# Performance work log

Hardware: AMD Instinct MI355X
Metric: run time of the kernel (lower is better)

## Reference

```python
import jax, jax.numpy as jnp
import numpy as np

N = 100000   # nodes
E = 640000   # edges
G = 256      # graphs in batch
L = 3        # mpnn layers
D_IN = 64    # in_node_channels
E_IN = 16    # in_edge_channels
H = 128      # hidden width (uniform)


def setup_inputs() -> dict:
    key = jax.random.key(0)
    ks = jax.random.split(key, 20)
    s = 0.05
    inp = {
        "x": jax.random.normal(ks[0], (N, D_IN), dtype=jnp.float32),
        "edge_index": jax.random.randint(ks[1], (2, E), 0, N, dtype=jnp.int64),
        "edge_attr": jax.random.normal(ks[2], (E, E_IN), dtype=jnp.float32),
        "batch_vec": jnp.sort(jax.random.randint(ks[3], (N,), 0, G, dtype=jnp.int64)),
        # input encoders
        "Wn0": jax.random.normal(ks[4], (D_IN, H), dtype=jnp.float32) * s,
        "bn0": jnp.zeros((H,), jnp.float32),
        "We0": jax.random.normal(ks[5], (E_IN, H), dtype=jnp.float32) * s,
        "be0": jnp.zeros((H,), jnp.float32),
        # per-layer MPNN params (stacked over L)
        "WM": jax.random.normal(ks[6], (L, 3 * H, H), dtype=jnp.float32) * s,
        "bM": jnp.zeros((L, H), jnp.float32),
        "WU": jax.random.normal(ks[7], (L, 2 * H, H), dtype=jnp.float32) * s,
        "bU": jnp.zeros((L, H), jnp.float32),
        # per-layer node/edge linear layers
        "Wn": jax.random.normal(ks[8], (L, H, H), dtype=jnp.float32) * s,
        "bn": jnp.zeros((L, H), jnp.float32),
        "We": jax.random.normal(ks[9], (L, H, H), dtype=jnp.float32) * s,
        "be": jnp.zeros((L, H), jnp.float32),
        "Wh": jax.random.normal(ks[10], (H, 1), dtype=jnp.float32) * s,
        "bh": jnp.zeros((1,), jnp.float32),
    }
    return inp


def _mpnn_layer(x, edge_attr, src, dst, WM, bM, WU, bU):
    # message: relu(Linear([x_i, x_j, e]))  (x_i = target, x_j = source)
    xi = x[dst]                                   # [E, H]
    xj = x[src]                                   # [E, H]
    m = jax.nn.relu(jnp.concatenate([xi, xj, edge_attr], axis=-1) @ WM + bM)
    # mean aggregation at target nodes
    agg = jax.ops.segment_sum(m, dst, num_segments=N)        # [N, H]
    cnt = jax.ops.segment_sum(jnp.ones((m.shape[0], 1), x.dtype), dst,
                              num_segments=N)
    agg = agg / jnp.maximum(cnt, 1.0)
    # update: relu(Linear([x, aggr_out]))
    return jax.nn.relu(jnp.concatenate([x, agg], axis=-1) @ WU + bU)


def reference(x, edge_index, edge_attr, batch_vec,
              Wn0, bn0, We0, be0, WM, bM, WU, bU, Wn, bn, We, be, Wh, bh):
    src, dst = edge_index[0], edge_index[1]       # PyG source_to_target flow
    h = jax.nn.relu(x @ Wn0 + bn0)                # NodeFeatureLinear
    e = jax.nn.relu(edge_attr @ We0 + be0)        # EdgeFeatureLinear
    for i in range(L):
        h = _mpnn_layer(h, e, src, dst, WM[i], bM[i], WU[i], bU[i])
        h = jax.nn.relu(h @ Wn[i] + bn[i])
        e = jax.nn.relu(e @ We[i] + be[i])
    # global mean pool over graphs
    sums = jax.ops.segment_sum(h, batch_vec, num_segments=G)  # [G, H]
    cnts = jax.ops.segment_sum(jnp.ones((N, 1), h.dtype), batch_vec,
                               num_segments=G)
    pooled = sums / jnp.maximum(cnts, 1.0)
    return pooled @ Wh + bh                       # [G, 1]
```

## Files before the change

### kernel.cpp

```cpp
#include <hip/hip_runtime.h>

#define NN 100000
#define EE 640000
#define GG 256
#define LL 3
#define HH 128

constexpr int BM = 64;
constexpr int BK = 16;

typedef _Float16 f16;
typedef f16 f16x8 __attribute__((ext_vector_type(8)));
typedef f16 f16x4 __attribute__((ext_vector_type(4)));
typedef f16 f16x2 __attribute__((ext_vector_type(2)));
typedef float f32x4 __attribute__((ext_vector_type(4)));

#define TSTR 136

__device__ __forceinline__ void gload_lds16(const void* g, void* l) {
  __builtin_amdgcn_global_load_lds(
      (const __attribute__((address_space(1))) void*)g,
      (__attribute__((address_space(3))) void*)l, 16, 0, 0);
}

template <int MODE>
__global__ __launch_bounds__(256) void gemm_k(
    const float* __restrict__ X, const float* __restrict__ W,
    const float* __restrict__ bias, float* __restrict__ out, int M, int K,
    const float* __restrict__ X2, const float* __restrict__ inv) {
  __shared__ __align__(16) float Xs[BK][BM];
  __shared__ __align__(16) float Ws[BK][HH];

  const int tid = threadIdx.x;
  const int m0 = blockIdx.x * BM;
  const int tm = (tid >> 4) << 2;
  const int tn = (tid & 15) << 3;
  const int xr = tid >> 2;
  const int xc = (tid & 3) << 2;

  float acc[4][8];
#pragma unroll
  for (int i = 0; i < 4; ++i)
#pragma unroll
    for (int j = 0; j < 8; ++j) acc[i][j] = 0.f;

  for (int k0 = 0; k0 < K; k0 += BK) {
    float4 xv = make_float4(0.f, 0.f, 0.f, 0.f);
    if (m0 + xr < M) {
      if (MODE == 3) {
        if (k0 < HH) {
          xv = *(const float4*)(X + (size_t)(m0 + xr) * HH + k0 + xc);
        } else {
          xv = *(const float4*)(X2 + (size_t)(m0 + xr) * HH + (k0 - HH) + xc);
          const float s = inv[m0 + xr];
          xv.x *= s; xv.y *= s; xv.z *= s; xv.w *= s;
        }
      } else {
        xv = *(const float4*)(X + (size_t)(m0 + xr) * K + k0 + xc);
      }
    }
    Xs[xc + 0][xr] = xv.x;
    Xs[xc + 1][xr] = xv.y;
    Xs[xc + 2][xr] = xv.z;
    Xs[xc + 3][xr] = xv.w;
#pragma unroll
    for (int i = 0; i < 2; ++i) {
      const int q = tid + i * 256;
      const int row = q >> 5;
      const int c4 = (q & 31) << 2;
      *(float4*)&Ws[row][c4] =
          *(const float4*)(W + (size_t)(k0 + row) * HH + c4);
    }
    __syncthreads();
#pragma unroll
    for (int k = 0; k < BK; ++k) {
      const float4 x4 = *(const float4*)&Xs[k][tm];
      const float4 w0 = *(const float4*)&Ws[k][tn];
      const float4 w1 = *(const float4*)&Ws[k][tn + 4];
      const float xr_[4] = {x4.x, x4.y, x4.z, x4.w};
      const float wr_[8] = {w0.x, w0.y, w0.z, w0.w, w1.x, w1.y, w1.z, w1.w};
#pragma unroll
      for (int i = 0; i < 4; ++i)
#pragma unroll
        for (int j = 0; j < 8; ++j)
          acc[i][j] = fmaf(xr_[i], wr_[j], acc[i][j]);
    }
    __syncthreads();
  }

#pragma unroll
  for (int i = 0; i < 4; ++i) {
    const int r = m0 + tm + i;
    if (r >= M) continue;
    float o[8];
#pragma unroll
    for (int j = 0; j < 8; ++j) {
      float v = acc[i][j];
      if (MODE == 1 || MODE == 3) {
        v += bias[tn + j];
        v = v > 0.f ? v : 0.f;
      }
      o[j] = v;
    }
    float4* d4 = (float4*)(out + (size_t)r * HH + tn);
    d4[0] = make_float4(o[0], o[1], o[2], o[3]);
    d4[1] = make_float4(o[4], o[5], o[6], o[7]);
  }
}

__global__ void prep_w(const float* __restrict__ We0,
                       const float* __restrict__ We,
                       const float* __restrict__ WM,
                       const float* __restrict__ Wn0,
                       const float* __restrict__ Wn,
                       const float* __restrict__ WU, f16* __restrict__ out) {
  const int buf = blockIdx.x >> 3;
  const int rowg = blockIdx.x & 7;
  const float* src;
  int K;
  if (buf == 0) {
    src = We0; K = 16;
  } else if (buf <= 2) {
    src = We + (size_t)(buf - 1) * HH * HH; K = HH;
  } else if (buf <= 5) {
    src = WM + (size_t)(buf - 3) * 3 * HH * HH + 2 * HH * HH; K = HH;
  } else if (buf == 6) {
    src = Wn0; K = 64;
  } else if (buf <= 9) {
    src = WM + (size_t)(buf - 7) * 3 * HH * HH; K = HH;
  } else if (buf <= 12) {
    src = WM + (size_t)(buf - 10) * 3 * HH * HH + HH * HH; K = HH;
  } else if (buf <= 15) {
    src = Wn + (size_t)(buf - 13) * HH * HH; K = HH;
  } else {
    const int t = buf - 16;
    src = WU + (size_t)(t >> 1) * 2 * HH * HH + (size_t)(t & 1) * HH * HH;
    K = HH;
  }
  f16* dst = out + (size_t)buf * HH * TSTR;
  for (int idx = threadIdx.x; idx < 16 * TSTR; idx += 256) {
    const int n = rowg * 16 + idx / TSTR;
    const int k = idx % TSTR;
    const float v = (k < K) ? src[(size_t)k * HH + n] : 0.f;
    dst[(size_t)n * TSTR + k] = (f16)v;
  }
}

template <int MODE>
__global__ __launch_bounds__(256) void gemm_mfma(
    const float* __restrict__ X, const f16* __restrict__ WT,
    const float* __restrict__ bias, float* __restrict__ out, int M,
    const float* __restrict__ X2, const float* __restrict__ inv,
    const f16* __restrict__ WT2, float* __restrict__ out2) {
  __shared__ __align__(16) char smem[17408 + 34816];
  f16* Xs = (f16*)smem;
  f16* Wt = (f16*)(smem + 17408);
  float* V = (float*)(smem + 17408);

  const int tid = threadIdx.x;
  const int lane = tid & 63;
  const int wv = tid >> 6;
  const int l15 = lane & 15;
  const int q = lane >> 4;
  const int m0 = blockIdx.x * 64;

  f32x4 acc[4][2];
#pragma unroll
  for (int mi = 0; mi < 4; ++mi)
#pragma unroll
    for (int ni = 0; ni < 2; ++ni) {
      f32x4 z = {};
      acc[mi][ni] = z;
    }

  auto stageX = [&](const float* Xp, int stride, int KC, bool scale) {
    const int npr = KC >> 2;
    for (int i = tid; i < 64 * npr; i += 256) {
      const int row = i / npr;
      const int c4 = (i - row * npr) << 2;
      float4 v = make_float4(0.f, 0.f, 0.f, 0.f);
      if (m0 + row < M) {
        v = *(const float4*)(Xp + (size_t)(m0 + row) * stride + c4);
        if (scale) {
          const float s = inv[m0 + row];
          v.x *= s; v.y *= s; v.z *= s; v.w *= s;
        }
      }
      f16x4 hv;
      hv[0] = (f16)v.x; hv[1] = (f16)v.y; hv[2] = (f16)v.z; hv[3] = (f16)v.w;
      *(f16x4*)&Xs[(size_t)row * TSTR + c4] = hv;
    }
  };

  auto stageW = [&](const f16* Wg) {
    const char* g = (const char*)Wg;
    char* l = (char*)Wt;
#pragma unroll
    for (int i = 0; i < 8; ++i)
      gload_lds16(g + tid * 16 + i * 4096, l + tid * 16 + i * 4096);
    if (tid < 128) gload_lds16(g + tid * 16 + 32768, l + tid * 16 + 32768);
  };

  auto mfmaN = [&](f32x4 (&ac)[4][2], int nk) {
    for (int kk = 0; kk < nk; ++kk) {
      f16x8 a[4], b[2];
#pragma unroll
      for (int mi = 0; mi < 4; ++mi)
        a[mi] = *(const f16x8*)&Xs[(size_t)(mi * 16 + l15) * TSTR + kk * 32 +
                                   q * 8];
#pragma unroll
      for (int ni = 0; ni < 2; ++ni)
        b[ni] = *(const f16x8*)&Wt[(size_t)((wv * 2 + ni) * 16 + l15) * TSTR +
                                   kk * 32 + q * 8];
#pragma unroll
      for (int mi = 0; mi < 4; ++mi)
#pragma unroll
        for (int ni = 0; ni < 2; ++ni)
          ac[mi][ni] = __builtin_amdgcn_mfma_f32_16x16x32_f16(
              a[mi], b[ni], ac[mi][ni], 0, 0, 0);
    }
  };

  auto dumpV = [&](f32x4 (&ac)[4][2], const float* bp) {
    float bv0 = 0.f, bv1 = 0.f;
    if (bp) { bv0 = bp[wv * 32 + l15]; bv1 = bp[wv * 32 + 16 + l15]; }
#pragma unroll
    for (int mi = 0; mi < 4; ++mi)
#pragma unroll
      for (int ni = 0; ni < 2; ++ni)
#pragma unroll
        for (int rr = 0; rr < 4; ++rr) {
          float v = ac[mi][ni][rr];
          if (bp) {
            v += ni ? bv1 : bv0;
            v = v > 0.f ? v : 0.f;
          }
          V[(size_t)(mi * 16 + q * 4 + rr) * 132 + wv * 32 + ni * 16 + l15] =
              v;
        }
  };

  auto storeV = [&](float* op) {
    const int tm = (tid >> 4) << 2;
    const int tn = (tid & 15) << 3;
#pragma unroll
    for (int i = 0; i < 4; ++i) {
      const int r = m0 + tm + i;
      if (r >= M) continue;
      float4* d = (float4*)(op + (size_t)r * HH + tn);
      d[0] = *(const float4*)&V[(size_t)(tm + i) * 132 + tn];
      d[1] = *(const float4*)&V[(size_t)(tm + i) * 132 + tn + 4];
    }
  };

  auto storeV16 = [&](f16* op) {
    const int tm = (tid >> 4) << 2;
    const int tn = (tid & 15) << 3;
#pragma unroll
    for (int i = 0; i < 4; ++i) {
      const int r = m0 + tm + i;
      if (r >= M) continue;
      const float* vp = &V[(size_t)(tm + i) * 132 + tn];
      f16x8 hv;
#pragma unroll
      for (int j = 0; j < 8; ++j) hv[j] = (f16)vp[j];
      *(f16x8*)(op + (size_t)r * HH + tn) = hv;
    }
  };

  if constexpr (MODE == 2) {
    stageW(WT);
    stageX(X, 64, 64, false);
    __syncthreads();
    mfmaN(acc, 2);
    __syncthreads();
    dumpV(acc, bias);
    __syncthreads();
    storeV(out);
  } else if constexpr (MODE == 1) {
    stageW(WT);
    stageX(X, HH, 128, false);
    __syncthreads();
    mfmaN(acc, 4);
    __syncthreads();
    dumpV(acc, bias);
    __syncthreads();
    storeV(out);
  } else if constexpr (MODE == 3) {
    stageW(WT);
    stageX(X, HH, 128, false);
    __syncthreads();
    mfmaN(acc, 4);
    __syncthreads();
    stageW(WT + (size_t)HH * TSTR);
    stageX(X2, HH, 128, true);
    __syncthreads();
    mfmaN(acc, 4);
    __syncthreads();
    dumpV(acc, bias);
    __syncthreads();
    storeV(out);
  } else {
    f32x4 acc2[4][2];
#pragma unroll
    for (int mi = 0; mi < 4; ++mi)
#pragma unroll
      for (int ni = 0; ni < 2; ++ni) {
        f32x4 z = {};
        acc2[mi][ni] = z;
      }
    stageW(WT);
    stageX(X, HH, 128, false);
    __syncthreads();
    mfmaN(acc, 4);
    __syncthreads();
    stageW(WT2);
    __syncthreads();
    mfmaN(acc2, 4);
    __syncthreads();
    dumpV(acc, nullptr);
    __syncthreads();
    storeV16((f16*)out);
    __syncthreads();
    dumpV(acc2, nullptr);
    __syncthreads();
    storeV16((f16*)out2);
  }
}

template <int CHAIN>
__global__ __launch_bounds__(512) void msg_k(
    const float* __restrict__ ea, const f16* __restrict__ W0T,
    const float* __restrict__ be0, const f16* __restrict__ WeT,
    const float* __restrict__ beL, const f16* __restrict__ WMeT,
    const float* __restrict__ bMl, const f16* __restrict__ A,
    const f16* __restrict__ B, const int* __restrict__ sIdx,
    const int* __restrict__ sSrc, const int* __restrict__ sDst,
    float* __restrict__ agg) {
  __shared__ __align__(16) char smem[34816 + 34816 + 512];
  f16* Tc = (f16*)smem;
  f16* Wc = (f16*)(smem + 34816);
  float* V = (float*)smem;
  int* dstS = (int*)(smem + 69632);

  const int tid = threadIdx.x;
  const int lane = tid & 63;
  const int wv = tid >> 6;
  const int ew = (wv >> 2) * 64;
  const int wn = wv & 3;
  const int l15 = lane & 15;
  const int q = lane >> 4;
  const int r0 = blockIdx.x * 128;

  auto wptr = [&](int p) -> const f16* {
    if (p == 0) return W0T;
    if (p <= CHAIN) return WeT + (size_t)(p - 1) * HH * TSTR;
    return WMeT;
  };

  auto stage_w = [&](const f16* Wg) {
    const char* g = (const char*)Wg;
    char* l = (char*)Wc;
#pragma unroll
    for (int i = 0; i < 4; ++i)
      gload_lds16(g + tid * 16 + i * 8192, l + tid * 16 + i * 8192);
    if (tid < 128) gload_lds16(g + tid * 16 + 32768, l + tid * 16 + 32768);
  };

  stage_w(wptr(0));
  {
    const int xr = tid >> 2;
    const int xc = (tid & 3) << 2;
    const int e = sIdx[r0 + xr];
    const float4 v = *(const float4*)(ea + (size_t)e * 16 + xc);
    f16x4 hv;
    hv[0] = (f16)v.x; hv[1] = (f16)v.y; hv[2] = (f16)v.z; hv[3] = (f16)v.w;
    *(f16x4*)&Tc[(size_t)xr * TSTR + xc] = hv;
    f16x4 z = {};
    *(f16x4*)&Tc[(size_t)xr * TSTR + 16 + xc] = z;
    if (tid < 128) dstS[tid] = sDst[r0 + tid];
  }

  f32x4 acc[4][2];

  auto zero_acc = [&]() {
#pragma unroll
    for (int mi = 0; mi < 4; ++mi)
#pragma unroll
      for (int ni = 0; ni < 2; ++ni) {
        f32x4 z = {};
        acc[mi][ni] = z;
      }
  };

  auto mfma_steps = [&](int nk) {
    for (int kk = 0; kk < nk; ++kk) {
      f16x8 a[4], b[2];
#pragma unroll
      for (int mi = 0; mi < 4; ++mi)
        a[mi] = *(const f16x8*)&Tc[(size_t)(ew + mi * 16 + l15) * TSTR +
                                   kk * 32 + q * 8];
#pragma unroll
      for (int ni = 0; ni < 2; ++ni)
        b[ni] = *(const f16x8*)&Wc[(size_t)((wn * 2 + ni) * 16 + l15) * TSTR +
                                   kk * 32 + q * 8];
#pragma unroll
      for (int mi = 0; mi < 4; ++mi)
#pragma unroll
        for (int ni = 0; ni < 2; ++ni)
          acc[mi][ni] = __builtin_amdgcn_mfma_f32_16x16x32_f16(
              a[mi], b[ni], acc[mi][ni], 0, 0, 0);
    }
  };

  auto relu_body = [&](const float* bias) {
    float bv0 = bias[wn * 32 + l15];
    float bv1 = bias[wn * 32 + 16 + l15];
#pragma unroll
    for (int mi = 0; mi < 4; ++mi)
#pragma unroll
      for (int ni = 0; ni < 2; ++ni) {
        const float bb = ni ? bv1 : bv0;
#pragma unroll
        for (int rr = 0; rr < 4; ++rr) {
          float v = acc[mi][ni][rr] + bb;
          v = v > 0.f ? v : 0.f;
          Tc[(size_t)(ew + mi * 16 + q * 4 + rr) * TSTR + wn * 32 + ni * 16 +
             l15] = (f16)v;
        }
      }
  };

  zero_acc();
  __syncthreads();
  mfma_steps(1);
  __syncthreads();
  stage_w(wptr(1));
  relu_body(be0);
  __syncthreads();

#pragma unroll
  for (int s = 0; s < CHAIN; ++s) {
    zero_acc();
    mfma_steps(4);
    __syncthreads();
    stage_w(wptr(s + 2));
    relu_body(beL + (size_t)s * HH);
    __syncthreads();
  }

  zero_acc();
  mfma_steps(4);
  __syncthreads();

#pragma unroll
  for (int mi = 0; mi < 4; ++mi)
#pragma unroll
    for (int ni = 0; ni < 2; ++ni)
#pragma unroll
      for (int rr = 0; rr < 4; ++rr)
        V[(size_t)(ew + mi * 16 + q * 4 + rr) * 129 + wn * 32 + ni * 16 +
          l15] = acc[mi][ni][rr];
  __syncthreads();

  const int tm = (tid >> 4) << 2;
  const int tn = (tid & 15) << 3;
  const float4 m0v = *(const float4*)(bMl + tn);
  const float4 m1v = *(const float4*)(bMl + tn + 4);
  const float mv[8] = {m0v.x, m0v.y, m0v.z, m0v.w,
                       m1v.x, m1v.y, m1v.z, m1v.w};
#pragma unroll
  for (int i = 0; i < 4; ++i) {
    const int rr = r0 + tm + i;
    const int d = dstS[tm + i];
    const int s = sSrc[rr];
    const f16x8 a8 = *(const f16x8*)(A + (size_t)d * HH + tn);
    const f16x8 b8 = *(const f16x8*)(B + (size_t)s * HH + tn);
    float* vp = &V[(size_t)(tm + i) * 129 + tn];
#pragma unroll
    for (int j = 0; j < 8; ++j)
      vp[j] = fmaxf(vp[j] + (float)a8[j] + (float)b8[j] + mv[j], 0.f);
  }
  __syncthreads();

  const int c = tid & 127;
  const int h = tid >> 7;
  float racc = 0.f;
  int cur = dstS[h * 32];
  bool first = true;
  for (int e2 = h * 32; e2 < h * 32 + 32; ++e2) {
    const int d = dstS[e2];
    if (d != cur) {
      if (first) {
        atomicAdd(&agg[(size_t)cur * HH + c], racc);
        first = false;
      } else {
        agg[(size_t)cur * HH + c] = racc;
      }
      racc = 0.f;
      cur = d;
    }
    racc += V[(size_t)e2 * 129 + c];
  }
  atomicAdd(&agg[(size_t)cur * HH + c], racc);
}

__global__ void count_kernel(const int* __restrict__ dst, int* cnt, int E) {
  const int i = blockIdx.x * 256 + threadIdx.x;
  if (i < E) atomicAdd(&cnt[dst[i]], 1);
}

__global__ void invcnt_kernel(const int* __restrict__ cnt, float* inv, int n) {
  const int i = blockIdx.x * 256 + threadIdx.x;
  if (i < n) inv[i] = 1.0f / (float)max(cnt[i], 1);
}

__global__ void scan_block(const int* __restrict__ cnt, int* excl, int* bsum,
                           int n) {
  __shared__ int s[256];
  const int tx = threadIdx.x;
  const int i = blockIdx.x * 256 + tx;
  const int v = (i < n) ? cnt[i] : 0;
  s[tx] = v;
  __syncthreads();
  for (int off = 1; off < 256; off <<= 1) {
    int tv = (tx >= off) ? s[tx - off] : 0;
    __syncthreads();
    s[tx] += tv;
    __syncthreads();
  }
  if (i < n) excl[i] = s[tx] - v;
  if (tx == 255) bsum[blockIdx.x] = s[255];
}

__global__ __launch_bounds__(512) void scan_bsum(int* bsum, int nb) {
  __shared__ int s[512];
  const int t = threadIdx.x;
  const int v0 = (t < nb) ? bsum[t] : 0;
  s[t] = v0;
  __syncthreads();
  for (int off = 1; off < 512; off <<= 1) {
    const int tv = (t >= off) ? s[t - off] : 0;
    __syncthreads();
    s[t] += tv;
    __syncthreads();
  }
  if (t < nb) bsum[t] = s[t] - v0;
}

__global__ void scan_add(int* excl, const int* __restrict__ bsum, int n) {
  const int i = blockIdx.x * 256 + threadIdx.x;
  if (i < n) excl[i] += bsum[blockIdx.x];
}

__global__ void scatter_edges(const int* __restrict__ dst,
                              const int* __restrict__ src,
                              const int* __restrict__ off, int* ctr, int* sIdx,
                              int* sSrc, int* sDst, int E) {
  const int e = blockIdx.x * 256 + threadIdx.x;
  if (e >= E) return;
  const int d = dst[e];
  const int p = off[d] + atomicAdd(&ctr[d], 1);
  sIdx[p] = e;
  sSrc[p] = src[e];
  sDst[p] = d;
}

__global__ void pool_accum(const float* __restrict__ h,
                           const int* __restrict__ batch,
                           float* __restrict__ gsum, int M) {
  const int col = threadIdx.x;
  const int r0 = blockIdx.x * 64;
  const int rend = min(r0 + 64, M);
  if (r0 >= M) return;
  float acc = 0.f;
  int cur = batch[r0];
  for (int r = r0; r < rend; ++r) {
    const int b = batch[r];
    if (b != cur) {
      atomicAdd(&gsum[(size_t)cur * HH + col], acc);
      acc = 0.f;
      cur = b;
    }
    acc += h[(size_t)r * HH + col];
  }
  atomicAdd(&gsum[(size_t)cur * HH + col], acc);
}

__global__ void gcnt_kernel(const int* __restrict__ batch, int* gcnt, int n) {
  const int i = blockIdx.x * 256 + threadIdx.x;
  if (i < n) atomicAdd(&gcnt[batch[i]], 1);
}

__global__ void head_kernel(const float* __restrict__ gsum,
                            const int* __restrict__ gcnt,
                            const float* __restrict__ Wh,
                            const float* __restrict__ bh,
                            float* __restrict__ out) {
  const int g = blockIdx.x;
  const int t = threadIdx.x;
  float v = gsum[(size_t)g * HH + t] * Wh[t];
#pragma unroll
  for (int o = 32; o > 0; o >>= 1) v += __shfl_down(v, o, 64);
  __shared__ float red[2];
  if ((t & 63) == 0) red[t >> 6] = v;
  __syncthreads();
  if (t == 0) {
    const float s = red[0] + red[1];
    const float c = (float)max(gcnt[g], 1);
    out[g] = s / c + bh[0];
  }
}

extern "C" void kernel_launch(void* const* d_in, const int* in_sizes, int n_in,
                              void* d_out, int out_size, void* d_ws,
                              size_t ws_size, hipStream_t stream) {
  (void)in_sizes; (void)n_in; (void)out_size;
  const float* x = (const float*)d_in[0];
  const int* ei = (const int*)d_in[1];
  const float* ea = (const float*)d_in[2];
  const int* batch = (const int*)d_in[3];
  const float* Wn0 = (const float*)d_in[4];
  const float* bn0 = (const float*)d_in[5];
  const float* We0 = (const float*)d_in[6];
  const float* be0 = (const float*)d_in[7];
  const float* WM = (const float*)d_in[8];
  const float* bM = (const float*)d_in[9];
  const float* WU = (const float*)d_in[10];
  const float* bU = (const float*)d_in[11];
  const float* Wn = (const float*)d_in[12];
  const float* bn = (const float*)d_in[13];
  const float* We = (const float*)d_in[14];
  const float* be = (const float*)d_in[15];
  const float* Wh = (const float*)d_in[16];
  const float* bh = (const float*)d_in[17];

  const int* srcI = ei;
  const int* dstI = ei + EE;

  float* w = (float*)d_ws;
  size_t o = 0;
  float* h = w + o;    o += (size_t)NN * HH;
  float* agg = w + o;  o += (size_t)NN * HH;
  f16* A16 = (f16*)(w + o); o += (size_t)NN * HH / 2;
  f16* B16 = (f16*)(w + o); o += (size_t)NN * HH / 2;
  float* gsum = w + o; o += (size_t)GG * HH;
  float* invc = w + o; o += (size_t)NN;
  int* cnt = (int*)(w + o);  o += (size_t)NN;
  int* gcnt = (int*)(w + o); o += (size_t)GG;
  int* off = (int*)(w + o);  o += (size_t)NN;
  int* ctr = (int*)(w + o);  o += (size_t)NN;
  int* bsum = (int*)(w + o); o += 512;
  int* sIdx = (int*)(w + o); o += (size_t)EE;
  int* sSrc = (int*)(w + o); o += (size_t)EE;
  int* sDst = (int*)(w + o); o += (size_t)EE;
  f16* Wp = (f16*)(w + o);   o += (size_t)22 * HH * TSTR / 2;
  if (o * sizeof(float) > ws_size) return;

  auto WB = [&](int i) { return Wp + (size_t)i * HH * TSTR; };

  const dim3 blk(256);
  const int gridN = (NN + BM - 1) / BM;
  const int gridE = EE / 128;
  const int NBLK = (NN + 255) / 256;

  hipMemsetAsync(cnt, 0, (size_t)NN * sizeof(int), stream);
  hipMemsetAsync(ctr, 0, (size_t)NN * sizeof(int), stream);
  hipMemsetAsync(gsum, 0, (size_t)GG * HH * sizeof(float), stream);
  hipMemsetAsync(gcnt, 0, (size_t)GG * sizeof(int), stream);

  count_kernel<<<(EE + 255) / 256, blk, 0, stream>>>(dstI, cnt, EE);
  scan_block<<<NBLK, blk, 0, stream>>>(cnt, off, bsum, NN);
  scan_bsum<<<1, dim3(512), 0, stream>>>(bsum, NBLK);
  scan_add<<<NBLK, blk, 0, stream>>>(off, bsum, NN);
  scatter_edges<<<(EE + 255) / 256, blk, 0, stream>>>(dstI, srcI, off, ctr,
                                                      sIdx, sSrc, sDst, EE);
  invcnt_kernel<<<(NN + 255) / 256, blk, 0, stream>>>(cnt, invc, NN);
  prep_w<<<22 * 8, blk, 0, stream>>>(We0, We, WM, Wn0, Wn, WU, Wp);

  gemm_mfma<2><<<gridN, blk, 0, stream>>>(x, WB(6), bn0, h, NN, nullptr,
                                          nullptr, nullptr, nullptr);

  for (int l = 0; l < LL; ++l) {
    gemm_mfma<4><<<gridN, blk, 0, stream>>>(h, WB(7 + l), nullptr,
                                            (float*)A16, NN, nullptr, nullptr,
                                            WB(10 + l), (float*)B16);
    hipMemsetAsync(agg, 0, (size_t)NN * HH * sizeof(float), stream);
    switch (l) {
      case 0:
        msg_k<0><<<gridE, dim3(512), 0, stream>>>(
            ea, WB(0), be0, WB(1), be, WB(3), bM + 0 * HH, A16, B16, sIdx,
            sSrc, sDst, agg);
        break;
      case 1:
        msg_k<1><<<gridE, dim3(512), 0, stream>>>(
            ea, WB(0), be0, WB(1), be, WB(4), bM + 1 * HH, A16, B16, sIdx,
            sSrc, sDst, agg);
        break;
      default:
        msg_k<2><<<gridE, dim3(512), 0, stream>>>(
            ea, WB(0), be0, WB(1), be, WB(5), bM + 2 * HH, A16, B16, sIdx,
            sSrc, sDst, agg);
        break;
    }
    gemm_mfma<3><<<gridN, blk, 0, stream>>>(h, WB(16 + 2 * l), bU + l * HH, h,
                                            NN, agg, invc, nullptr, nullptr);
    gemm_mfma<1><<<gridN, blk, 0, stream>>>(h, WB(13 + l), bn + l * HH, h, NN,
                                            nullptr, nullptr, nullptr,
                                            nullptr);
  }

  pool_accum<<<gridN, dim3(128), 0, stream>>>(h, batch, gsum, NN);
  gcnt_kernel<<<(NN + 255) / 256, blk, 0, stream>>>(batch, gcnt, NN);
  head_kernel<<<GG, dim3(128), 0, stream>>>(gsum, gcnt, Wh, bh, (float*)d_out);
}
```

Baseline: 1.121 ms.

## Double-buffer message-kernel weights, widen block to 256 edges, store messages in fp16

The message kernel now double-buffers the weight tiles in LDS, so the next layer's weights load while the current MFMA chain runs instead of after a barrier. Each block doubles to 1024 threads covering 256 edges, and the per-edge message scratch is kept in fp16 with the padded stride instead of fp32. The goal is to hide the weight-staging latency and cut barrier stalls and LDS traffic. In exchange, LDS use per block grows to about 140KB, which allows only one block per CU, and messages lose precision before aggregation.

```diff
diff --git a/kernel.cpp b/kernel.cpp
--- a/kernel.cpp
+++ b/kernel.cpp
@@ -329,7 +329,7 @@
 }
 
 template <int CHAIN>
-__global__ __launch_bounds__(512) void msg_k(
+__global__ __launch_bounds__(1024) void msg_k(
     const float* __restrict__ ea, const f16* __restrict__ W0T,
     const float* __restrict__ be0, const f16* __restrict__ WeT,
     const float* __restrict__ beL, const f16* __restrict__ WMeT,
@@ -337,11 +337,11 @@
     const f16* __restrict__ B, const int* __restrict__ sIdx,
     const int* __restrict__ sSrc, const int* __restrict__ sDst,
     float* __restrict__ agg) {
-  __shared__ __align__(16) char smem[34816 + 34816 + 512];
+  __shared__ __align__(16) char smem[69632 + 34816 + 34816 + 1024];
   f16* Tc = (f16*)smem;
-  f16* Wc = (f16*)(smem + 34816);
-  float* V = (float*)smem;
-  int* dstS = (int*)(smem + 69632);
+  f16* WcB = (f16*)(smem + 69632);
+  f16* V16 = (f16*)smem;
+  int* dstS = (int*)(smem + 139264);
 
   const int tid = threadIdx.x;
   const int lane = tid & 63;
@@ -350,7 +350,7 @@
   const int wn = wv & 3;
   const int l15 = lane & 15;
   const int q = lane >> 4;
-  const int r0 = blockIdx.x * 128;
+  const int r0 = blockIdx.x * 256;
 
   auto wptr = [&](int p) -> const f16* {
     if (p == 0) return W0T;
@@ -358,16 +358,16 @@
     return WMeT;
   };
 
-  auto stage_w = [&](const f16* Wg) {
+  auto stage_w = [&](int b, const f16* Wg) {
     const char* g = (const char*)Wg;
-    char* l = (char*)Wc;
-#pragma unroll
-    for (int i = 0; i < 4; ++i)
-      gload_lds16(g + tid * 16 + i * 8192, l + tid * 16 + i * 8192);
+    char* l = (char*)(WcB + (size_t)b * HH * TSTR);
+#pragma unroll
+    for (int i = 0; i < 2; ++i)
+      gload_lds16(g + tid * 16 + i * 16384, l + tid * 16 + i * 16384);
     if (tid < 128) gload_lds16(g + tid * 16 + 32768, l + tid * 16 + 32768);
   };
 
-  stage_w(wptr(0));
+  stage_w(0, wptr(0));
   {
     const int xr = tid >> 2;
     const int xc = (tid & 3) << 2;
@@ -378,7 +378,7 @@
     *(f16x4*)&Tc[(size_t)xr * TSTR + xc] = hv;
     f16x4 z = {};
     *(f16x4*)&Tc[(size_t)xr * TSTR + 16 + xc] = z;
-    if (tid < 128) dstS[tid] = sDst[r0 + tid];
+    if (tid < 256) dstS[tid] = sDst[r0 + tid];
   }
 
   f32x4 acc[4][2];
@@ -393,23 +393,24 @@
       }
   };
 
-  auto mfma_steps = [&](int nk) {
+  auto mfma_steps = [&](int b, int nk) {
+    const f16* Wc = WcB + (size_t)b * HH * TSTR;
     for (int kk = 0; kk < nk; ++kk) {
-      f16x8 a[4], b[2];
+      f16x8 a[4], bb[2];
 #pragma unroll
       for (int mi = 0; mi < 4; ++mi)
         a[mi] = *(const f16x8*)&Tc[(size_t)(ew + mi * 16 + l15) * TSTR +
                                    kk * 32 + q * 8];
 #pragma unroll
       for (int ni = 0; ni < 2; ++ni)
-        b[ni] = *(const f16x8*)&Wc[(size_t)((wn * 2 + ni) * 16 + l15) * TSTR +
-                                   kk * 32 + q * 8];
+        bb[ni] = *(const f16x8*)&Wc[(size_t)((wn * 2 + ni) * 16 + l15) * TSTR +
+                                    kk * 32 + q * 8];
 #pragma unroll
       for (int mi = 0; mi < 4; ++mi)
 #pragma unroll
         for (int ni = 0; ni < 2; ++ni)
           acc[mi][ni] = __builtin_amdgcn_mfma_f32_16x16x32_f16(
-              a[mi], b[ni], acc[mi][ni], 0, 0, 0);
+              a[mi], bb[ni], acc[mi][ni], 0, 0, 0);
     }
   };
 
@@ -433,24 +434,24 @@
 
   zero_acc();
   __syncthreads();
-  mfma_steps(1);
-  __syncthreads();
-  stage_w(wptr(1));
+  stage_w(1, wptr(1));
+  mfma_steps(0, 1);
+  __syncthreads();
   relu_body(be0);
   __syncthreads();
 
 #pragma unroll
   for (int s = 0; s < CHAIN; ++s) {
     zero_acc();
-    mfma_steps(4);
-    __syncthreads();
-    stage_w(wptr(s + 2));
+    stage_w((s + 2) & 1, wptr(s + 2));
+    mfma_steps((s + 1) & 1, 4);
+    __syncthreads();
     relu_body(beL + (size_t)s * HH);
     __syncthreads();
   }
 
   zero_acc();
-  mfma_steps(4);
+  mfma_steps((CHAIN + 1) & 1, 4);
   __syncthreads();
 
 #pragma unroll
@@ -459,8 +460,8 @@
     for (int ni = 0; ni < 2; ++ni)
 #pragma unroll
       for (int rr = 0; rr < 4; ++rr)
-        V[(size_t)(ew + mi * 16 + q * 4 + rr) * 129 + wn * 32 + ni * 16 +
-          l15] = acc[mi][ni][rr];
+        V16[(size_t)(ew + mi * 16 + q * 4 + rr) * TSTR + wn * 32 + ni * 16 +
+            l15] = (f16)acc[mi][ni][rr];
   __syncthreads();
 
   const int tm = (tid >> 4) << 2;
@@ -476,10 +477,14 @@
     const int s = sSrc[rr];
     const f16x8 a8 = *(const f16x8*)(A + (size_t)d * HH + tn);
     const f16x8 b8 = *(const f16x8*)(B + (size_t)s * HH + tn);
-    float* vp = &V[(size_t)(tm + i) * 129 + tn];
+    f16* vp = &V16[(size_t)(tm + i) * TSTR + tn];
+    const f16x8 pv = *(const f16x8*)vp;
+    f16x8 o;
 #pragma unroll
     for (int j = 0; j < 8; ++j)
-      vp[j] = fmaxf(vp[j] + (float)a8[j] + (float)b8[j] + mv[j], 0.f);
+      o[j] = (f16)fmaxf((float)pv[j] + (float)a8[j] + (float)b8[j] + mv[j],
+                        0.f);
+    *(f16x8*)vp = o;
   }
   __syncthreads();
 
@@ -500,7 +505,7 @@
       racc = 0.f;
       cur = d;
     }
-    racc += V[(size_t)e2 * 129 + c];
+    racc += (float)V16[(size_t)e2 * TSTR + c];
   }
   atomicAdd(&agg[(size_t)cur * HH + c], racc);
 }
@@ -661,7 +666,7 @@
 
   const dim3 blk(256);
   const int gridN = (NN + BM - 1) / BM;
-  const int gridE = EE / 128;
+  const int gridE = EE / 256;
   const int NBLK = (NN + 255) / 256;
 
   hipMemsetAsync(cnt, 0, (size_t)NN * sizeof(int), stream);
@@ -688,17 +693,17 @@
     hipMemsetAsync(agg, 0, (size_t)NN * HH * sizeof(float), stream);
     switch (l) {
       case 0:
-        msg_k<0><<<gridE, dim3(512), 0, stream>>>(
+        msg_k<0><<<gridE, dim3(1024), 0, stream>>>(
             ea, WB(0), be0, WB(1), be, WB(3), bM + 0 * HH, A16, B16, sIdx,
             sSrc, sDst, agg);
         break;
       case 1:
-        msg_k<1><<<gridE, dim3(512), 0, stream>>>(
+        msg_k<1><<<gridE, dim3(1024), 0, stream>>>(
             ea, WB(0), be0, WB(1), be, WB(4), bM + 1 * HH, A16, B16, sIdx,
             sSrc, sDst, agg);
         break;
       default:
-        msg_k<2><<<gridE, dim3(512), 0, stream>>>(
+        msg_k<2><<<gridE, dim3(1024), 0, stream>>>(
             ea, WB(0), be0, WB(1), be, WB(5), bM + 2 * HH, A16, B16, sIdx,
             sSrc, sDst, agg);
         break;
```

Measured after the change: 1.146 ms. 1.02x slower.
